# Kernel tuning notes

Hardware: AMD Instinct MI355X
Metric: run time of the kernel (lower is better)

The kernel has to match this reference:

```python
import jax, jax.numpy as jnp
import numpy as np

B, C, E, H = 8, 2048, 1024, 128


def setup_inputs() -> dict:
    key = jax.random.key(0)
    kx, kq, kk, kv = jax.random.split(key, 4)
    scale = 1.0 / np.sqrt(E)
    return {
        "x": jax.random.normal(kx, (B, C, E), dtype=jnp.float32),
        "Wq": jax.random.normal(kq, (E, H), dtype=jnp.float32) * scale,
        "Wk": jax.random.normal(kk, (E, H), dtype=jnp.float32) * scale,
        "Wv": jax.random.normal(kv, (E, H), dtype=jnp.float32) * scale,
    }


def reference(x, Wq, Wk, Wv):
    # x: (B, C, E); projections -> (B, C, H)
    q = jnp.einsum("bce,eh->bch", x, Wq)
    k = jnp.einsum("bce,eh->bch", x, Wk)
    v = jnp.einsum("bce,eh->bch", x, Wv)
    # NOTE: original scales by sqrt(embed_size), not head_size
    scores = jnp.einsum("bqh,bkh->bqk", q, k) / jnp.sqrt(jnp.asarray(E, x.dtype))
    Cq = x.shape[1]
    causal = jnp.tril(jnp.ones((Cq, Cq), dtype=bool))
    scores = jnp.where(causal, scores, -jnp.inf)
    weights = jax.nn.softmax(scores, axis=-1)  # (B, C, C)
    out = jnp.einsum("bqk,bkh->bqh", weights, v)
    return out
```

## Files before the change

### kernel.cpp

```cpp
#include <hip/hip_runtime.h>
#include <hip/hip_bf16.h>

#define BATCH 8
#define CTX   2048
#define EMB   1024
#define HD    128
#define VSTR  2080

using bf16x8 = __attribute__((ext_vector_type(8))) short;
using fx4    = __attribute__((ext_vector_type(4))) float;

__device__ __forceinline__ ushort f2bf(float f) {
    union { float f; unsigned u; } v; v.f = f;
    unsigned u = v.u;
    u += 0x7fffu + ((u >> 16) & 1u);
    return (ushort)(u >> 16);
}

__device__ __forceinline__ unsigned cvtpk(float a, float b) {
    unsigned r;
    asm("v_cvt_pk_bf16_f32 %0, %1, %2" : "=v"(r) : "v"(a), "v"(b));
    return r;
}

__device__ __forceinline__ void gload16(const void* g, void* l) {
    __builtin_amdgcn_global_load_lds(
        (const __attribute__((address_space(1))) unsigned*)g,
        (__attribute__((address_space(3))) unsigned*)l, 16, 0, 0);
}

__global__ void wt_kernel(const float* __restrict__ Wq, const float* __restrict__ Wk,
                          const float* __restrict__ Wv, ushort* __restrict__ Wt) {
    int idx = blockIdx.x * blockDim.x + threadIdx.x;
    int e = idx % EMB;
    int h = (idx / EMB) % HD;
    int w = idx / (EMB * HD);
    const float* W = (w == 0) ? Wq : (w == 1) ? Wk : Wv;
    Wt[idx] = f2bf(W[e * HD + h]);
}

__global__ __launch_bounds__(256) void proj_kernel(
        const float* __restrict__ x, const ushort* __restrict__ Wt,
        ushort* __restrict__ q, ushort* __restrict__ k, ushort* __restrict__ vt) {
    __shared__ __align__(16) float  As[128 * 64];
    __shared__ __align__(16) ushort Bs[128 * 64];

    const int t    = threadIdx.x;
    const int wave = t >> 6;
    const int lane = t & 63;
    const int lo = lane & 15, hi = lane >> 4;
    const int wr = wave >> 1, wc = wave & 1;
    const int bn   = blockIdx.x;
    const int brow = blockIdx.y * 128;

    const char* Ab = (const char*)As;
    const char* Bb = (const char*)Bs;

    fx4 acc[4][4];
#pragma unroll
    for (int m2 = 0; m2 < 4; m2++)
#pragma unroll
        for (int n = 0; n < 4; n++) acc[m2][n] = fx4{0.f, 0.f, 0.f, 0.f};

    const int arow_s = t >> 4;
    const int acol_s = ((t & 15) ^ ((t >> 4) & 7)) << 2;
    const int brow_s = t >> 3;
    const int bcol_s = ((t & 7) ^ ((t >> 3) & 7)) << 3;
    const int ldsbase = wave * 1024;

    for (int k0 = 0; k0 < EMB; k0 += 64) {
#pragma unroll
        for (int r = 0; r < 8; r++)
            gload16(x + (size_t)(brow + r * 16 + arow_s) * EMB + k0 + acol_s,
                    (char*)As + r * 4096 + ldsbase);
#pragma unroll
        for (int r = 0; r < 4; r++)
            gload16(Wt + (size_t)(bn * 128 + r * 32 + brow_s) * EMB + k0 + bcol_s,
                    (char*)Bs + r * 4096 + ldsbase);
        __syncthreads();

#pragma unroll
        for (int ks = 0; ks < 2; ks++) {
            bf16x8 af[4], bfr[4];
#pragma unroll
            for (int m2 = 0; m2 < 4; m2++) {
                const int rowA = wr * 64 + m2 * 16 + lo;
                const unsigned sw = (rowA & 7) << 4;
                const unsigned ub = rowA * 256 + ks * 128 + hi * 32;
                fx4 a0 = *(const fx4*)(Ab + (ub ^ sw));
                fx4 a1 = *(const fx4*)(Ab + ((ub + 16) ^ sw));
                union { unsigned u[4]; bf16x8 v; } pk;
                pk.u[0] = cvtpk(a0[0], a0[1]);
                pk.u[1] = cvtpk(a0[2], a0[3]);
                pk.u[2] = cvtpk(a1[0], a1[1]);
                pk.u[3] = cvtpk(a1[2], a1[3]);
                af[m2] = pk.v;
            }
#pragma unroll
            for (int n = 0; n < 4; n++) {
                const int rowB = wc * 64 + n * 16 + lo;
                const unsigned ub = rowB * 128 + ks * 64 + hi * 16;
                bfr[n] = *(const bf16x8*)(Bb + (ub ^ ((rowB & 7) << 4)));
            }
#pragma unroll
            for (int m2 = 0; m2 < 4; m2++)
#pragma unroll
                for (int n = 0; n < 4; n++)
                    acc[m2][n] = __builtin_amdgcn_mfma_f32_16x16x32_bf16(af[m2], bfr[n], acc[m2][n], 0, 0, 0);
        }
        __syncthreads();
    }

    const float qscale = 0.03125f;
#pragma unroll
    for (int m2 = 0; m2 < 4; m2++) {
#pragma unroll
        for (int n = 0; n < 4; n++) {
            const int c = wc * 64 + n * 16 + lo;
#pragma unroll
            for (int j = 0; j < 4; j++) {
                const int r = brow + wr * 64 + m2 * 16 + hi * 4 + j;
                if (bn == 0)      q[(size_t)r * HD + c] = f2bf(acc[m2][n][j] * qscale);
                else if (bn == 1) k[(size_t)r * HD + c] = f2bf(acc[m2][n][j]);
                else {
                    const int bb = r >> 11, cc = r & (CTX - 1);
                    vt[((size_t)bb * HD + c) * VSTR + cc] = f2bf(acc[m2][n][j]);
                }
            }
        }
    }
}

__global__ __launch_bounds__(128) void attn_kernel(
        const ushort* __restrict__ q, const ushort* __restrict__ k,
        const ushort* __restrict__ vt, float* __restrict__ out) {
    __shared__ __align__(16) char Ks[16384];
    __shared__ __align__(16) char Vs[16384];
    __shared__ __align__(16) char p_lds[2][1024];

    const int id   = blockIdx.x;
    const int b    = id & 7;
    const int pos  = id >> 3;
    const int qt   = 127 - pos;
    const int q0   = qt * 16;
    const int t    = threadIdx.x;
    const int w    = t >> 6;
    const int lane = t & 63;
    const int lo = lane & 15, hi = lane >> 4;

    const ushort* qb = q  + (size_t)b * CTX * HD;
    const ushort* kb = k  + (size_t)b * CTX * HD;
    const ushort* vb = vt + (size_t)b * HD * VSTR;

    bf16x8 qf[4];
#pragma unroll
    for (int ks = 0; ks < 4; ks++)
        qf[ks] = *(const bf16x8*)(qb + (q0 + lo) * HD + ks * 32 + hi * 8);

    fx4 o[8];
#pragma unroll
    for (int h = 0; h < 8; h++) o[h] = fx4{0.f, 0.f, 0.f, 0.f};
    float m[4], l[4];
#pragma unroll
    for (int j = 0; j < 4; j++) { m[j] = 0.f; l[j] = 0.f; }

    const int krow = t >> 4;
    const int ksl  = ((t & 15) ^ (krow & 7)) << 3;
    const int vrow = t >> 3;
    const int vsl  = ((t & 7) ^ (vrow & 7)) << 3;

    const int nkv = qt / 4 + 1;
    for (int it = 0; it < nkv; ++it) {
        const int kv0 = it * 64;
        __builtin_amdgcn_s_barrier();
#pragma unroll
        for (int r = 0; r < 8; ++r)
            gload16(kb + (size_t)(kv0 + r * 8 + krow) * HD + ksl,
                    Ks + r * 2048 + w * 1024);
#pragma unroll
        for (int r = 0; r < 8; ++r)
            gload16(vb + (size_t)(r * 16 + vrow) * VSTR + kv0 + vsl,
                    Vs + r * 2048 + w * 1024);
        asm volatile("s_waitcnt vmcnt(0)" ::: "memory");
        __builtin_amdgcn_sched_barrier(0);
        __builtin_amdgcn_s_barrier();
        __builtin_amdgcn_sched_barrier(0);

        fx4 s[2];
        s[0] = fx4{0.f, 0.f, 0.f, 0.f};
        s[1] = fx4{0.f, 0.f, 0.f, 0.f};
        __builtin_amdgcn_s_setprio(1);
#pragma unroll
        for (int n2 = 0; n2 < 2; n2++) {
            const int row = w * 32 + n2 * 16 + lo;
            const unsigned sw = (unsigned)((row & 7) << 4);
#pragma unroll
            for (int ks = 0; ks < 4; ks++) {
                bf16x8 kf = *(const bf16x8*)(Ks + row * 256 + ((ks * 64 + hi * 16) ^ sw));
                s[n2] = __builtin_amdgcn_mfma_f32_16x16x32_bf16(qf[ks], kf, s[n2], 0, 0, 0);
            }
        }
        __builtin_amdgcn_s_setprio(0);

        const bool diag = (kv0 + 64 > q0);
        float pmax[4];
        int allok = 1;
#pragma unroll
        for (int j = 0; j < 4; j++) {
            const int r = q0 + hi * 4 + j;
            if (diag) {
#pragma unroll
                for (int n2 = 0; n2 < 2; n2++)
                    if ((kv0 + w * 32 + n2 * 16 + lo) > r) s[n2][j] = -INFINITY;
            }
            pmax[j] = fmaxf(s[0][j], s[1][j]);
            allok &= (pmax[j] <= m[j] + 16.0f);
        }
        if (!__all(allok)) {
#pragma unroll
            for (int j = 0; j < 4; j++) {
                float mx = pmax[j];
                mx = fmaxf(mx, __shfl_xor(mx, 1));
                mx = fmaxf(mx, __shfl_xor(mx, 2));
                mx = fmaxf(mx, __shfl_xor(mx, 4));
                mx = fmaxf(mx, __shfl_xor(mx, 8));
                const float mn = fmaxf(m[j], mx);
                const float f  = __expf(m[j] - mn);
                l[j] *= f;
#pragma unroll
                for (int h = 0; h < 8; h++) o[h][j] *= f;
                m[j] = mn;
            }
        }
#pragma unroll
        for (int j = 0; j < 4; j++) {
            float sum = 0.f;
#pragma unroll
            for (int n2 = 0; n2 < 2; n2++) {
                const float pv = __expf(s[n2][j] - m[j]);
                s[n2][j] = pv;
                sum += pv;
            }
            l[j] += sum;
            const int row = hi * 4 + j;
            const unsigned sw = (unsigned)((row & 3) << 4);
#pragma unroll
            for (int n2 = 0; n2 < 2; n2++) {
                const unsigned cb = (unsigned)((n2 * 16 + lo) * 2);
                *(ushort*)(p_lds[w] + row * 64 + (cb ^ sw)) = f2bf(s[n2][j]);
            }
        }
        asm volatile("" ::: "memory");
        bf16x8 pa = *(const bf16x8*)(p_lds[w] + lo * 64 + ((hi * 16) ^ ((lo & 3) << 4)));
        __builtin_amdgcn_s_setprio(1);
#pragma unroll
        for (int h = 0; h < 8; h++) {
            const int vr = h * 16 + lo;
            bf16x8 vf = *(const bf16x8*)(Vs + vr * 128 + ((w * 64 + hi * 16) ^ ((vr & 7) << 4)));
            o[h] = __builtin_amdgcn_mfma_f32_16x16x32_bf16(pa, vf, o[h], 0, 0, 0);
        }
        __builtin_amdgcn_s_setprio(0);
    }

#pragma unroll
    for (int j = 0; j < 4; j++) {
        l[j] += __shfl_xor(l[j], 1);
        l[j] += __shfl_xor(l[j], 2);
        l[j] += __shfl_xor(l[j], 4);
        l[j] += __shfl_xor(l[j], 8);
    }

    float* oB = (float*)Ks;
    float* mlB = (float*)Vs;
    __syncthreads();
    if (w == 1) {
#pragma unroll
        for (int j = 0; j < 4; j++) {
            const int row = hi * 4 + j;
            if (lo == 0) { mlB[row] = m[j]; mlB[16 + row] = l[j]; }
#pragma unroll
            for (int h = 0; h < 8; h++) oB[row * 128 + h * 16 + lo] = o[h][j];
        }
    }
    __syncthreads();
    if (w == 0) {
        float* ob = out + ((size_t)b * CTX + q0) * HD;
#pragma unroll
        for (int j = 0; j < 4; j++) {
            const int row = hi * 4 + j;
            const float mB = mlB[row], lB = mlB[16 + row];
            const float mt = fmaxf(m[j], mB);
            const float fA = __expf(m[j] - mt);
            const float fB = __expf(mB - mt);
            const float inv = 1.0f / (l[j] * fA + lB * fB);
#pragma unroll
            for (int h = 0; h < 8; h++)
                ob[row * HD + h * 16 + lo] =
                    (o[h][j] * fA + oB[row * 128 + h * 16 + lo] * fB) * inv;
        }
    }
}

extern "C" void kernel_launch(void* const* d_in, const int* in_sizes, int n_in,
                              void* d_out, int out_size, void* d_ws, size_t ws_size,
                              hipStream_t stream) {
    const float* x  = (const float*)d_in[0];
    const float* Wq = (const float*)d_in[1];
    const float* Wk = (const float*)d_in[2];
    const float* Wv = (const float*)d_in[3];

    ushort* Wt = (ushort*)d_ws;
    ushort* qw = (ushort*)((char*)d_ws + 786432);
    ushort* kw = qw + (size_t)BATCH * CTX * HD;
    ushort* vw = kw + (size_t)BATCH * CTX * HD;

    wt_kernel<<<(3 * HD * EMB) / 256, 256, 0, stream>>>(Wq, Wk, Wv, Wt);
    proj_kernel<<<dim3(3, 128), 256, 0, stream>>>(x, Wt, qw, kw, vw);
    attn_kernel<<<1024, 128, 0, stream>>>(qw, kw, vw, (float*)d_out);
}
```

Baseline: 101.8 us.

## Double-buffer LDS loads in projection and attention, retile projection to fused QKV

Measured after the change: 100.6 us. No clear change (-1.2%).

```diff
diff --git a/kernel.cpp b/kernel.cpp
--- a/kernel.cpp
+++ b/kernel.cpp
@@ -42,89 +42,102 @@
 __global__ __launch_bounds__(256) void proj_kernel(
         const float* __restrict__ x, const ushort* __restrict__ Wt,
         ushort* __restrict__ q, ushort* __restrict__ k, ushort* __restrict__ vt) {
-    __shared__ __align__(16) float  As[128 * 64];
-    __shared__ __align__(16) ushort Bs[128 * 64];
+    __shared__ __align__(16) char As[2][4096];
+    __shared__ __align__(16) char Bs[2][24576];
 
     const int t    = threadIdx.x;
     const int wave = t >> 6;
     const int lane = t & 63;
     const int lo = lane & 15, hi = lane >> 4;
-    const int wr = wave >> 1, wc = wave & 1;
-    const int bn   = blockIdx.x;
-    const int brow = blockIdx.y * 128;
-
-    const char* Ab = (const char*)As;
-    const char* Bb = (const char*)Bs;
-
-    fx4 acc[4][4];
-#pragma unroll
-    for (int m2 = 0; m2 < 4; m2++)
-#pragma unroll
-        for (int n = 0; n < 4; n++) acc[m2][n] = fx4{0.f, 0.f, 0.f, 0.f};
-
-    const int arow_s = t >> 4;
-    const int acol_s = ((t & 15) ^ ((t >> 4) & 7)) << 2;
-    const int brow_s = t >> 3;
-    const int bcol_s = ((t & 7) ^ ((t >> 3) & 7)) << 3;
-    const int ldsbase = wave * 1024;
-
-    for (int k0 = 0; k0 < EMB; k0 += 64) {
-#pragma unroll
-        for (int r = 0; r < 8; r++)
-            gload16(x + (size_t)(brow + r * 16 + arow_s) * EMB + k0 + acol_s,
-                    (char*)As + r * 4096 + ldsbase);
-#pragma unroll
-        for (int r = 0; r < 4; r++)
-            gload16(Wt + (size_t)(bn * 128 + r * 32 + brow_s) * EMB + k0 + bcol_s,
-                    (char*)Bs + r * 4096 + ldsbase);
-        __syncthreads();
-
-#pragma unroll
-        for (int ks = 0; ks < 2; ks++) {
-            bf16x8 af[4], bfr[4];
-#pragma unroll
-            for (int m2 = 0; m2 < 4; m2++) {
-                const int rowA = wr * 64 + m2 * 16 + lo;
-                const unsigned sw = (rowA & 7) << 4;
-                const unsigned ub = rowA * 256 + ks * 128 + hi * 32;
-                fx4 a0 = *(const fx4*)(Ab + (ub ^ sw));
-                fx4 a1 = *(const fx4*)(Ab + ((ub + 16) ^ sw));
-                union { unsigned u[4]; bf16x8 v; } pk;
-                pk.u[0] = cvtpk(a0[0], a0[1]);
-                pk.u[1] = cvtpk(a0[2], a0[3]);
-                pk.u[2] = cvtpk(a1[0], a1[1]);
-                pk.u[3] = cvtpk(a1[2], a1[3]);
-                af[m2] = pk.v;
-            }
-#pragma unroll
-            for (int n = 0; n < 4; n++) {
-                const int rowB = wc * 64 + n * 16 + lo;
-                const unsigned ub = rowB * 128 + ks * 64 + hi * 16;
-                bfr[n] = *(const bf16x8*)(Bb + (ub ^ ((rowB & 7) << 4)));
-            }
-#pragma unroll
-            for (int m2 = 0; m2 < 4; m2++)
-#pragma unroll
-                for (int n = 0; n < 4; n++)
-                    acc[m2][n] = __builtin_amdgcn_mfma_f32_16x16x32_bf16(af[m2], bfr[n], acc[m2][n], 0, 0, 0);
-        }
-        __syncthreads();
-    }
+    const int brow = blockIdx.x * 32;
+
+    fx4 acc[2][6];
+#pragma unroll
+    for (int m2 = 0; m2 < 2; m2++)
+#pragma unroll
+        for (int n = 0; n < 6; n++) acc[m2][n] = fx4{0.f, 0.f, 0.f, 0.f};
+
+    const int arow  = t >> 3;
+    const int aslot = (t & 7) ^ (arow & 7);
+    const float* asrc = x + (size_t)(brow + arow) * EMB + aslot * 4;
+
+    const ushort* bsrc[6];
+#pragma unroll
+    for (int r = 0; r < 6; r++) {
+        const int lrow = r * 32 + (t >> 3);
+        const int u    = (t & 7) ^ (lrow & 7);
+        bsrc[r] = Wt + (size_t)(lrow * 2 + (u >> 2)) * EMB + (u & 3) * 8;
+    }
+
+#define PSTAGE(bi, k0_) do {                                          \
+    gload16(asrc + (k0_), As[bi] + wave * 1024);                      \
+    _Pragma("unroll")                                                 \
+    for (int r = 0; r < 6; ++r)                                       \
+        gload16(bsrc[r] + (k0_), Bs[bi] + r * 4096 + wave * 1024);    \
+} while (0)
+
+    PSTAGE(0, 0);
+    for (int it = 0; it < 32; ++it) {
+        if (it + 1 < 32) {
+            PSTAGE((it + 1) & 1, (it + 1) * 32);
+            asm volatile("s_waitcnt vmcnt(7)" ::: "memory");
+        } else {
+            asm volatile("s_waitcnt vmcnt(0)" ::: "memory");
+        }
+        __builtin_amdgcn_sched_barrier(0);
+        __builtin_amdgcn_s_barrier();
+        __builtin_amdgcn_sched_barrier(0);
+
+        const char* Ab = As[it & 1];
+        const char* Bb = Bs[it & 1];
+
+        bf16x8 af[2];
+#pragma unroll
+        for (int m2 = 0; m2 < 2; m2++) {
+            const int rowA = m2 * 16 + lo;
+            const int s0 = (hi * 2) ^ (rowA & 7);
+            const int s1 = (hi * 2 + 1) ^ (rowA & 7);
+            fx4 a0 = *(const fx4*)(Ab + rowA * 128 + s0 * 16);
+            fx4 a1 = *(const fx4*)(Ab + rowA * 128 + s1 * 16);
+            union { unsigned u[4]; bf16x8 v; } pk;
+            pk.u[0] = cvtpk(a0[0], a0[1]);
+            pk.u[1] = cvtpk(a0[2], a0[3]);
+            pk.u[2] = cvtpk(a1[0], a1[1]);
+            pk.u[3] = cvtpk(a1[2], a1[3]);
+            af[m2] = pk.v;
+        }
+        __builtin_amdgcn_s_setprio(1);
+#pragma unroll
+        for (int n = 0; n < 6; n++) {
+            const int col  = wave * 96 + n * 16 + lo;
+            const int rowp = col >> 1;
+            const int slot = ((col & 1) * 4 + hi) ^ (rowp & 7);
+            bf16x8 bfr = *(const bf16x8*)(Bb + rowp * 128 + slot * 16);
+#pragma unroll
+            for (int m2 = 0; m2 < 2; m2++)
+                acc[m2][n] = __builtin_amdgcn_mfma_f32_16x16x32_bf16(af[m2], bfr, acc[m2][n], 0, 0, 0);
+        }
+        __builtin_amdgcn_s_setprio(0);
+        __builtin_amdgcn_s_barrier();
+    }
+#undef PSTAGE
 
     const float qscale = 0.03125f;
 #pragma unroll
-    for (int m2 = 0; m2 < 4; m2++) {
-#pragma unroll
-        for (int n = 0; n < 4; n++) {
-            const int c = wc * 64 + n * 16 + lo;
+    for (int n = 0; n < 6; n++) {
+        const int col = wave * 96 + n * 16 + lo;
+        const int bnn = col >> 7;
+        const int cc  = col & 127;
+#pragma unroll
+        for (int m2 = 0; m2 < 2; m2++) {
 #pragma unroll
             for (int j = 0; j < 4; j++) {
-                const int r = brow + wr * 64 + m2 * 16 + hi * 4 + j;
-                if (bn == 0)      q[(size_t)r * HD + c] = f2bf(acc[m2][n][j] * qscale);
-                else if (bn == 1) k[(size_t)r * HD + c] = f2bf(acc[m2][n][j]);
+                const int r = brow + m2 * 16 + hi * 4 + j;
+                if (bnn == 0)      q[(size_t)r * HD + cc] = f2bf(acc[m2][n][j] * qscale);
+                else if (bnn == 1) k[(size_t)r * HD + cc] = f2bf(acc[m2][n][j]);
                 else {
-                    const int bb = r >> 11, cc = r & (CTX - 1);
-                    vt[((size_t)bb * HD + c) * VSTR + cc] = f2bf(acc[m2][n][j]);
+                    const int bb = r >> 11, ccc = r & (CTX - 1);
+                    vt[((size_t)bb * HD + cc) * VSTR + ccc] = f2bf(acc[m2][n][j]);
                 }
             }
         }
@@ -134,8 +147,8 @@
 __global__ __launch_bounds__(128) void attn_kernel(
         const ushort* __restrict__ q, const ushort* __restrict__ k,
         const ushort* __restrict__ vt, float* __restrict__ out) {
-    __shared__ __align__(16) char Ks[16384];
-    __shared__ __align__(16) char Vs[16384];
+    __shared__ __align__(16) char Ks[2][16384];
+    __shared__ __align__(16) char Vs[2][16384];
     __shared__ __align__(16) char p_lds[2][1024];
 
     const int id   = blockIdx.x;
@@ -169,22 +182,33 @@
     const int vrow = t >> 3;
     const int vsl  = ((t & 7) ^ (vrow & 7)) << 3;
 
+#define STAGE(bi, kv0_) do {                                          \
+    _Pragma("unroll")                                                 \
+    for (int r = 0; r < 8; ++r)                                       \
+        gload16(kb + (size_t)((kv0_) + r * 8 + krow) * HD + ksl,      \
+                Ks[bi] + r * 2048 + w * 1024);                        \
+    _Pragma("unroll")                                                 \
+    for (int r = 0; r < 8; ++r)                                       \
+        gload16(vb + (size_t)(r * 16 + vrow) * VSTR + (kv0_) + vsl,   \
+                Vs[bi] + r * 2048 + w * 1024);                        \
+} while (0)
+
     const int nkv = qt / 4 + 1;
+    STAGE(0, 0);
     for (int it = 0; it < nkv; ++it) {
-        const int kv0 = it * 64;
-        __builtin_amdgcn_s_barrier();
-#pragma unroll
-        for (int r = 0; r < 8; ++r)
-            gload16(kb + (size_t)(kv0 + r * 8 + krow) * HD + ksl,
-                    Ks + r * 2048 + w * 1024);
-#pragma unroll
-        for (int r = 0; r < 8; ++r)
-            gload16(vb + (size_t)(r * 16 + vrow) * VSTR + kv0 + vsl,
-                    Vs + r * 2048 + w * 1024);
-        asm volatile("s_waitcnt vmcnt(0)" ::: "memory");
+        if (it + 1 < nkv) {
+            STAGE((it + 1) & 1, (it + 1) * 64);
+            asm volatile("s_waitcnt vmcnt(16)" ::: "memory");
+        } else {
+            asm volatile("s_waitcnt vmcnt(0)" ::: "memory");
+        }
         __builtin_amdgcn_sched_barrier(0);
         __builtin_amdgcn_s_barrier();
         __builtin_amdgcn_sched_barrier(0);
+
+        const char* Kb = Ks[it & 1];
+        const char* Vb = Vs[it & 1];
+        const int kv0 = it * 64;
 
         fx4 s[2];
         s[0] = fx4{0.f, 0.f, 0.f, 0.f};
@@ -196,7 +220,7 @@
             const unsigned sw = (unsigned)((row & 7) << 4);
 #pragma unroll
             for (int ks = 0; ks < 4; ks++) {
-                bf16x8 kf = *(const bf16x8*)(Ks + row * 256 + ((ks * 64 + hi * 16) ^ sw));
+                bf16x8 kf = *(const bf16x8*)(Kb + row * 256 + ((ks * 64 + hi * 16) ^ sw));
                 s[n2] = __builtin_amdgcn_mfma_f32_16x16x32_bf16(qf[ks], kf, s[n2], 0, 0, 0);
             }
         }
@@ -256,11 +280,13 @@
 #pragma unroll
         for (int h = 0; h < 8; h++) {
             const int vr = h * 16 + lo;
-            bf16x8 vf = *(const bf16x8*)(Vs + vr * 128 + ((w * 64 + hi * 16) ^ ((vr & 7) << 4)));
+            bf16x8 vf = *(const bf16x8*)(Vb + vr * 128 + ((w * 64 + hi * 16) ^ ((vr & 7) << 4)));
             o[h] = __builtin_amdgcn_mfma_f32_16x16x32_bf16(pa, vf, o[h], 0, 0, 0);
         }
         __builtin_amdgcn_s_setprio(0);
-    }
+        __builtin_amdgcn_s_barrier();
+    }
+#undef STAGE
 
 #pragma unroll
     for (int j = 0; j < 4; j++) {
@@ -270,8 +296,8 @@
         l[j] += __shfl_xor(l[j], 8);
     }
 
-    float* oB = (float*)Ks;
-    float* mlB = (float*)Vs;
+    float* oB  = (float*)Ks[0];
+    float* mlB = (float*)Vs[0];
     __syncthreads();
     if (w == 1) {
 #pragma unroll
@@ -315,6 +341,6 @@
     ushort* vw = kw + (size_t)BATCH * CTX * HD;
 
     wt_kernel<<<(3 * HD * EMB) / 256, 256, 0, stream>>>(Wq, Wk, Wv, Wt);
-    proj_kernel<<<dim3(3, 128), 256, 0, stream>>>(x, Wt, qw, kw, vw);
+    proj_kernel<<<(BATCH * CTX) / 32, 256, 0, stream>>>(x, Wt, qw, kw, vw);
     attn_kernel<<<1024, 128, 0, stream>>>(qw, kw, vw, (float*)d_out);
 }
```
